# Performance work log

Measured on AMD Instinct MI355X. Metric: run time of the kernel, lower is better.

The kernel has to match this reference:

```python
import jax, jax.numpy as jnp
import numpy as np

N, E, U, L = 10000, 320000, 256, 3


def setup_inputs() -> dict:
    key = jax.random.key(0)
    ks = jax.random.split(key, 16)
    s = 0.05
    p = {}
    p["pos"] = jax.random.normal(ks[0], (N, 2), jnp.float32)
    p["edge_attr_in"] = jax.random.uniform(ks[1], (E, 1), jnp.float32)
    p["edge_index"] = jax.random.randint(ks[2], (2, E), 0, N)
    p["Wp"] = jax.random.normal(ks[3], (2, U), jnp.float32) * s
    p["bp"] = jnp.zeros((U,), jnp.float32)
    p["Wa"] = jax.random.normal(ks[4], (1, U), jnp.float32) * s
    p["ba"] = jnp.zeros((U,), jnp.float32)
    p["W1"] = jax.random.normal(ks[5], (L, U, U), jnp.float32) * s
    p["b1"] = jnp.zeros((L, U), jnp.float32)
    p["W2"] = jax.random.normal(ks[6], (L, U, U), jnp.float32) * s
    p["b2"] = jnp.zeros((L, U), jnp.float32)
    p["We"] = jax.random.normal(ks[7], (L + 1, U, U), jnp.float32) * s
    p["be"] = jnp.zeros((L + 1, U), jnp.float32)
    p["Ws"] = jax.random.normal(ks[8], (L + 1, U, U), jnp.float32) * s
    p["Wt"] = jax.random.normal(ks[9], (L + 1, U, U), jnp.float32) * s
    p["Wm1"] = jax.random.normal(ks[10], (U + 1, U // 2), jnp.float32) * s
    p["bm1"] = jnp.zeros((U // 2,), jnp.float32)
    p["alpha"] = 0.25 * jnp.ones((1,), jnp.float32)  # PReLU default slope
    p["Wm2"] = jax.random.normal(ks[11], (U // 2, 1), jnp.float32) * s
    p["bm2"] = jnp.zeros((1,), jnp.float32)
    return p


def _forward(pos, edge_attr_in, edge_index, Wp, bp, Wa, ba, W1, b1, W2, b2,
             We, be, Ws, Wt, Wm1, bm1, alpha, Wm2, bm2):
    src, dst = edge_index[0], edge_index[1]
    x = pos @ Wp + bp                      # [N, U]
    e = edge_attr_in @ Wa + ba             # [E, U]

    def edge_update(x, e, l):
        # ResEdgeLinear: residual edge update from endpoint nodes + edge feats
        return e + jax.nn.relu(e @ We[l] + x[src] @ Ws[l] + x[dst] @ Wt[l] + be[l])

    for l in range(L):
        # ResNodeConv: gated gather-linear-scatter with residual
        gate = jax.nn.sigmoid(e)                                   # [E, U]
        msg = gate * (x[src] @ W2[l] + b2[l])                      # [E, U]
        agg = jax.ops.segment_sum(msg, dst, num_segments=N)        # [N, U]
        x_new = x + jax.nn.relu(x @ W1[l] + b1[l] + agg)
        e_new = edge_update(x, e, l)  # simultaneous update: both use old (x, e)
        x, e = x_new, e_new
    e = edge_update(x, e, L)

    h = jnp.concatenate([e, edge_attr_in[:, :1]], axis=-1) @ Wm1 + bm1
    h = jnp.where(h > 0, h, alpha * h)  # PReLU
    return h @ Wm2 + bm2                # [E, 1] logits


def reference(pos, edge_attr_in, edge_index, Wp, bp, Wa, ba, W1, b1, W2, b2,
              We, be, Ws, Wt, Wm1, bm1, alpha, Wm2, bm2):
    return _forward(pos, edge_attr_in, edge_index, Wp, bp, Wa, ba, W1, b1,
                    W2, b2, We, be, Ws, Wt, Wm1, bm1, alpha, Wm2, bm2)
```

## Files before the change

### kernel.cpp

```cpp
#include <hip/hip_runtime.h>
#include <stdint.h>

#define N_NODES 10000
#define N_EDGES 320000

using bf16x8 = __attribute__((ext_vector_type(8))) short;
using fp32x4 = __attribute__((ext_vector_type(4))) float;
using u16x8 = __attribute__((ext_vector_type(8))) unsigned short;
using i32x4 = __attribute__((ext_vector_type(4))) int;

__device__ __forceinline__ float bf2f(unsigned short u) {
  union { unsigned int i; float f; } v; v.i = ((unsigned int)u) << 16; return v.f;
}
__device__ __forceinline__ unsigned short f2bf(float f) {
  union { float f; unsigned int i; } v; v.f = f;
  unsigned int x = v.i;
  x += 0x7fffu + ((x >> 16) & 1u);
  return (unsigned short)(x >> 16);
}

#define A_POS 0
#define A_EA 20000
#define A_WP 340000
#define A_BP 340512
#define A_WA 340768
#define A_BA 341024
#define A_W1 341280
#define A_B1 537888
#define A_W2 538656
#define A_B2 735264
#define A_WE 736032
#define A_BE 998176
#define A_WS 999200
#define A_WT 1261344
#define A_WM1 1523488
#define A_BM1 1556384
#define A_AL 1556512
#define A_WM2 1556544
#define A_BM2 1556672
#define ARENA_USED 1556673
#define ARENA_TOT 1556736

__constant__ int g_off[19] = {A_POS, A_EA, A_WP, A_BP, A_WA, A_BA, A_W1, A_B1,
                              A_W2, A_B2, A_WE, A_BE, A_WS, A_WT, A_WM1,
                              A_BM1, A_AL, A_WM2, A_BM2};

struct Ptrs { const void* p[19]; };

__global__ void k_detect(const unsigned short* wpraw, int* flag, int* deg) {
  int i = blockIdx.x * 256 + threadIdx.x;
  if (i < N_NODES) deg[i] = 0;
  if (blockIdx.x == 0) {
    __shared__ int cnt;
    int tid = threadIdx.x;
    if (tid == 0) cnt = 0;
    __syncthreads();
    float v0 = bf2f(wpraw[tid]);
    float v1 = bf2f(wpraw[256 + tid]);
    int big = (fabsf(v0) > 100.f ? 1 : 0) + (fabsf(v1) > 100.f ? 1 : 0);
    atomicAdd(&cnt, big);
    __syncthreads();
    if (tid == 0) *flag = (cnt > 10) ? 1 : 0;
  }
}

__global__ void k_cast(Ptrs ptrs, const int* __restrict__ flag,
                       unsigned short* __restrict__ arena) {
  int a = blockIdx.x * 256 + threadIdx.x;
  if (a >= ARENA_USED) return;
  int z = 0;
#pragma unroll
  for (int j = 1; j < 19; ++j) if (a >= g_off[j]) z = j;
  int i = a - g_off[z];
  float v;
  if (*flag) v = ((const float*)ptrs.p[z])[i];
  else       v = bf2f(((const unsigned short*)ptrs.p[z])[i]);
  arena[a] = f2bf(v);
}

__global__ void k_prep(const unsigned short* __restrict__ arena,
                       unsigned short* nodeBT, unsigned short* WeT,
                       unsigned short* Wm1T, unsigned short* biascat) {
  int z = blockIdx.z;
  int i = blockIdx.x * 256 + threadIdx.x;
  if (z == 19) {
    if (i < 3072) {
      int l = i >> 10, j = i & 1023;
      unsigned short v = 0;
      if (j < 256) v = arena[A_B1 + l * 256 + j];
      else if (j < 512) v = arena[A_B2 + l * 256 + (j - 256)];
      biascat[i] = v;
    } else if (i < 3584) {
      biascat[i] = 0;
    }
    return;
  }
  const unsigned short* src; unsigned short* dst; int srcN = 256;
  if (z < 3)       {                 src = arena + A_W1 + z * 65536; dst = nodeBT + z * 262144; }
  else if (z < 6)  { int l = z - 3;  src = arena + A_W2 + l * 65536; dst = nodeBT + l * 262144 + 65536; }
  else if (z < 10) { int l = z - 6;  src = arena + A_WS + l * 65536;
                     dst = (l < 3) ? nodeBT + l * 262144 + 131072 : nodeBT + 786432; }
  else if (z < 14) { int l = z - 10; src = arena + A_WT + l * 65536;
                     dst = (l < 3) ? nodeBT + l * 262144 + 196608 : nodeBT + 786432 + 65536; }
  else if (z < 18) { int l = z - 14; src = arena + A_WE + l * 65536; dst = WeT + l * 65536; }
  else             { src = arena + A_WM1; dst = Wm1T; srcN = 128; }
  if (i < srcN * 256) {
    int k = i & 255, n = i >> 8;
    dst[i] = src[k * srcN + n];
  }
}

__global__ void k_init_x(const unsigned short* __restrict__ arena,
                         float* __restrict__ xf, unsigned short* __restrict__ xbf,
                         float* __restrict__ agg) {
  int n = blockIdx.x, c = threadIdx.x;
  float p0 = bf2f(arena[A_POS + 2 * n]), p1 = bf2f(arena[A_POS + 2 * n + 1]);
  float v = fmaf(p0, bf2f(arena[A_WP + c]),
                 fmaf(p1, bf2f(arena[A_WP + 256 + c]), bf2f(arena[A_BP + c])));
  long idx = ((long)n << 8) + c;
  xf[idx] = v;
  xbf[idx] = f2bf(v);
  agg[idx] = 0.f;
}

__global__ void k_hist(const int* __restrict__ dstA, int* __restrict__ deg) {
  int i = blockIdx.x * 256 + threadIdx.x;
  if (i < N_EDGES) {
    int d = dstA[i];
    if ((unsigned)d < N_NODES) atomicAdd(&deg[d], 1);
  }
}

__global__ void k_scan(const int* __restrict__ deg, int* __restrict__ rowptr,
                       int* __restrict__ cursor) {
  __shared__ int part[256];
  int tid = threadIdx.x;
  int base = tid * 40;
  int s = 0;
  for (int i = 0; i < 40; ++i) {
    int idx = base + i;
    if (idx < N_NODES) s += deg[idx];
  }
  part[tid] = s;
  __syncthreads();
  if (tid == 0) {
    int run = 0;
    for (int i = 0; i < 256; ++i) { int t = part[i]; part[i] = run; run += t; }
    rowptr[N_NODES] = run;
  }
  __syncthreads();
  int run = part[tid];
  for (int i = 0; i < 40; ++i) {
    int idx = base + i;
    if (idx < N_NODES) { rowptr[idx] = run; cursor[idx] = run; run += deg[idx]; }
  }
}

__global__ void k_fill(const int* __restrict__ dstA, const int* __restrict__ srcA,
                       const unsigned short* __restrict__ arena,
                       int* __restrict__ cursor, int* __restrict__ eid,
                       int* __restrict__ csrc, int* __restrict__ cdst,
                       unsigned short* __restrict__ eaC) {
  int i = blockIdx.x * 256 + threadIdx.x;
  if (i < N_EDGES) {
    int d = dstA[i]; if ((unsigned)d >= N_NODES) d = 0;
    int p = atomicAdd(&cursor[d], 1);
    if ((unsigned)p < N_EDGES) {
      eid[p] = i;
      int s = srcA[i]; if ((unsigned)s >= N_NODES) s = 0;
      csrc[p] = s;
      cdst[p] = d;
      eaC[p] = arena[A_EA + i];
    }
  }
}

#define SM_PITCH 528
#define EDGE_BLOCKS (N_EDGES / 128)

template <bool NT, int ROWS>
__device__ __forceinline__ void stage_tile(char* smc, const unsigned short* src,
                                           long rowBase) {
  int tid = threadIdx.x;
#pragma unroll
  for (int it = 0; it < ROWS / 8; ++it) {
    int lin = it * 256 + tid;
    int row = lin >> 5, g = lin & 31;
    const i32x4* p = (const i32x4*)((const char*)src + ((rowBase + row) << 9) + (g << 4));
    i32x4 v = NT ? __builtin_nontemporal_load(p) : *p;
    *(i32x4*)(smc + row * SM_PITCH + (g << 4)) = v;
  }
}

template <int MT, int NTT>
__device__ __forceinline__ void gemm_swap(const char* smc, const unsigned short* WT,
                                          int colBase, fp32x4 (&acc)[MT][NTT]) {
  const int lane = threadIdx.x & 63;
  const int q = lane >> 4, ll = lane & 15;
  const int llperm = ((ll >> 2) * (MT * 4)) + (ll & 3);
#pragma unroll
  for (int ks = 0; ks < 8; ++ks) {
    bf16x8 a[MT];
#pragma unroll
    for (int mt = 0; mt < MT; ++mt) {
      int oc = colBase + llperm + mt * 4;
      a[mt] = *(const bf16x8*)((const char*)WT + ((long)oc << 9) + (ks << 6) + (q << 4));
    }
    bf16x8 b[NTT];
#pragma unroll
    for (int nt = 0; nt < NTT; ++nt)
      b[nt] = *(const bf16x8*)(smc + (nt * 16 + ll) * SM_PITCH + (ks << 6) + (q << 4));
#pragma unroll
    for (int mt = 0; mt < MT; ++mt)
#pragma unroll
      for (int nt = 0; nt < NTT; ++nt)
        acc[mt][nt] = __builtin_amdgcn_mfma_f32_16x16x32_bf16(a[mt], b[nt], acc[mt][nt], 0, 0, 0);
  }
}

template <int NTT>
__device__ __forceinline__ void edge_epilogue(
    char* smc, const fp32x4 (&acc)[4][NTT], const int* s_src, const int* s_dst,
    const unsigned short* XW, int xw_pitch, int xs_off, int xt_off,
    const unsigned short* bePtr, int cb, int ll) {
  u16x8 be0 = *(const u16x8*)(bePtr + cb);
  u16x8 be1 = *(const u16x8*)(bePtr + cb + 8);
#pragma unroll
  for (int nt = 0; nt < NTT; ++nt) {
    int el = nt * 16 + ll;
    int sn = s_src[el], dn = s_dst[el];
    const unsigned short* xsrow = XW + (long)sn * xw_pitch + xs_off + cb;
    const unsigned short* xtrow = XW + (long)dn * xw_pitch + xt_off + cb;
    u16x8 xs0 = *(const u16x8*)(xsrow);
    u16x8 xs1 = *(const u16x8*)(xsrow + 8);
    u16x8 xt0 = *(const u16x8*)(xtrow);
    u16x8 xt1 = *(const u16x8*)(xtrow + 8);
    u16x8* slot = (u16x8*)(smc + el * SM_PITCH + cb * 2);
    u16x8 er0 = slot[0], er1 = slot[1];
    u16x8 o0, o1;
#pragma unroll
    for (int mt = 0; mt < 4; ++mt)
#pragma unroll
      for (int r = 0; r < 4; ++r) {
        int i = mt * 4 + r;
        float xsv = bf2f(i < 8 ? xs0[i] : xs1[i - 8]);
        float xtv = bf2f(i < 8 ? xt0[i] : xt1[i - 8]);
        float erv = bf2f(i < 8 ? er0[i] : er1[i - 8]);
        float bev = bf2f(i < 8 ? be0[i] : be1[i - 8]);
        float v = acc[mt][nt][r] + xsv + xtv + bev;
        v = fmaxf(v, 0.f);
        unsigned short ob = f2bf(erv + v);
        if (i < 8) o0[i] = ob; else o1[i - 8] = ob;
      }
    slot[0] = o0;
    slot[1] = o1;
  }
}

template <int MODE>
__global__ __launch_bounds__(256, 2) void k_fat(
    unsigned short* __restrict__ e, const unsigned short* __restrict__ WT_edge,
    const unsigned short* __restrict__ XW_edge,
    const unsigned short* __restrict__ bePtr, const unsigned short* __restrict__ arena,
    const unsigned short* __restrict__ eaC,
    const int* __restrict__ csrc, const int* __restrict__ cdst,
    const unsigned short* __restrict__ xbf, const unsigned short* __restrict__ WT_node,
    const unsigned short* __restrict__ bias, unsigned short* __restrict__ XW_out) {
  __shared__ int4 sm4[128 * 33];
  __shared__ int s_src[128];
  __shared__ int s_dst[128];
  char* smc = (char*)sm4;
  const int tid = threadIdx.x;
  const int wave = tid >> 6, lane = tid & 63;
  const int q = lane >> 4, ll = lane & 15;

  if (blockIdx.x < EDGE_BLOCKS) {
    const long tileBase = (long)blockIdx.x * 128;
    const int colBase = wave * 64;
    if (MODE == 0) {
#pragma unroll
      for (int it = 0; it < 16; ++it) {
        int lin = it * 256 + tid;
        int row = lin >> 5, g = lin & 31;
        float eav = bf2f(eaC[tileBase + row]);
        int c0 = g * 8;
        bf16x8 ov;
#pragma unroll
        for (int j = 0; j < 8; ++j) {
          float f = fmaf(eav, bf2f(arena[A_WA + c0 + j]), bf2f(arena[A_BA + c0 + j]));
          ((unsigned short*)&ov)[j] = f2bf(f);
        }
        *(bf16x8*)(smc + row * SM_PITCH + (g << 4)) = ov;
      }
    } else {
      stage_tile<true, 128>(smc, e, tileBase);
    }
    if (tid < 128) {
      long edge = tileBase + tid;
      int s = csrc[edge]; if ((unsigned)s >= N_NODES) s = 0;
      int d = cdst[edge]; if ((unsigned)d >= N_NODES) d = 0;
      s_src[tid] = s;
      s_dst[tid] = d;
    }
    __syncthreads();

    fp32x4 acc[4][8];
#pragma unroll
    for (int mt = 0; mt < 4; ++mt)
#pragma unroll
      for (int nt = 0; nt < 8; ++nt) acc[mt][nt] = 0.f;
    gemm_swap<4, 8>(smc, WT_edge, colBase, acc);
    __syncthreads();

    edge_epilogue<8>(smc, acc, s_src, s_dst, XW_edge, 1024, 512, 768,
                     bePtr, colBase + q * 16, ll);
    __syncthreads();

#pragma unroll
    for (int it = 0; it < 16; ++it) {
      int lin = it * 256 + tid;
      int row = lin >> 5, g = lin & 31;
      i32x4 v = *(const i32x4*)(smc + row * SM_PITCH + (g << 4));
      __builtin_nontemporal_store(v, (i32x4*)((char*)e + ((tileBase + row) << 9) + (g << 4)));
    }
  } else {
    int b = blockIdx.x - EDGE_BLOCKS;
    int bx = b % 79, by = b / 79;
    const long tileBase = (long)bx * 128;
#pragma unroll
    for (int it = 0; it < 16; ++it) {
      int lin = it * 256 + tid;
      int row = lin >> 5, g = lin & 31;
      long rg = tileBase + row;
      if (rg > N_NODES - 1) rg = N_NODES - 1;
      i32x4 v = *(const i32x4*)((const char*)xbf + (rg << 9) + (g << 4));
      *(i32x4*)(smc + row * SM_PITCH + (g << 4)) = v;
    }
    __syncthreads();
    fp32x4 acc[2][8];
#pragma unroll
    for (int mt = 0; mt < 2; ++mt)
#pragma unroll
      for (int nt = 0; nt < 8; ++nt) acc[mt][nt] = 0.f;
    const int colBase = by * 128 + wave * 32;
    gemm_swap<2, 8>(smc, WT_node, colBase, acc);

    const int cb = colBase + q * 8;
    u16x8 bs8 = *(const u16x8*)(bias + cb);
#pragma unroll
    for (int nt = 0; nt < 8; ++nt) {
      long nn = tileBase + nt * 16 + ll;
      if (nn >= N_NODES) continue;
      u16x8 o0;
#pragma unroll
      for (int mt = 0; mt < 2; ++mt)
#pragma unroll
        for (int r = 0; r < 4; ++r) {
          int i = mt * 4 + r;
          o0[i] = f2bf(acc[mt][nt][r] + bf2f(bs8[i]));
        }
      *(u16x8*)(XW_out + nn * 1024 + cb) = o0;
    }
  }
}

__global__ __launch_bounds__(256, 2) void k_edge_last2(
    const unsigned short* __restrict__ e, const unsigned short* __restrict__ WeT2,
    const unsigned short* __restrict__ WeT3,
    const unsigned short* __restrict__ XW2, const unsigned short* __restrict__ XW3,
    const unsigned short* __restrict__ arena, const unsigned short* __restrict__ eaC,
    const int* __restrict__ csrc, const int* __restrict__ cdst,
    const unsigned short* __restrict__ Wm1T, const int* __restrict__ eid,
    const int* __restrict__ flag, void* __restrict__ out) {
  __shared__ int4 sm4[128 * 33];
  __shared__ int s_src[128];
  __shared__ int s_dst[128];
  char* smc = (char*)sm4;
  const long tileBase = (long)blockIdx.x * 128;
  const int tid = threadIdx.x;
  const int wave = tid >> 6, lane = tid & 63;
  const int q = lane >> 4, ll = lane & 15;
  const int colBase = wave * 64;

  stage_tile<true, 128>(smc, e, tileBase);
  if (tid < 128) {
    long edge = tileBase + tid;
    int s = csrc[edge]; if ((unsigned)s >= N_NODES) s = 0;
    int d = cdst[edge]; if ((unsigned)d >= N_NODES) d = 0;
    s_src[tid] = s;
    s_dst[tid] = d;
  }
  __syncthreads();

  fp32x4 acc[4][8];
#pragma unroll
  for (int mt = 0; mt < 4; ++mt)
#pragma unroll
    for (int nt = 0; nt < 8; ++nt) acc[mt][nt] = 0.f;
  gemm_swap<4, 8>(smc, WeT2, colBase, acc);
  __syncthreads();
  edge_epilogue<8>(smc, acc, s_src, s_dst, XW2, 1024, 512, 768,
                   arena + A_BE + 2 * 256, colBase + q * 16, ll);
  __syncthreads();

#pragma unroll
  for (int mt = 0; mt < 4; ++mt)
#pragma unroll
    for (int nt = 0; nt < 8; ++nt) acc[mt][nt] = 0.f;
  gemm_swap<4, 8>(smc, WeT3, colBase, acc);
  __syncthreads();
  edge_epilogue<8>(smc, acc, s_src, s_dst, XW3, 512, 0, 256,
                   arena + A_BE + 3 * 256, colBase + q * 16, ll);
  __syncthreads();

  fp32x4 acc2[2][8];
#pragma unroll
  for (int mt = 0; mt < 2; ++mt)
#pragma unroll
    for (int nt = 0; nt < 8; ++nt) acc2[mt][nt] = 0.f;
  const int colBase2 = wave * 32;
  gemm_swap<2, 8>(smc, Wm1T, colBase2, acc2);

  const int cb2 = colBase2 + q * 8;
  float alphaf = bf2f(arena[A_AL]);
  float bmc[8], wl[8], w2c[8];
#pragma unroll
  for (int i = 0; i < 8; ++i) {
    bmc[i] = bf2f(arena[A_BM1 + cb2 + i]);
    wl[i] = bf2f(arena[A_WM1 + 32768 + cb2 + i]);
    w2c[i] = bf2f(arena[A_WM2 + cb2 + i]);
  }
  __syncthreads();
  float* part = (float*)smc;
#pragma unroll
  for (int nt = 0; nt < 8; ++nt) {
    int el = nt * 16 + ll;
    float eav = bf2f(eaC[tileBase + el]);
    float ps = 0.f;
#pragma unroll
    for (int mt = 0; mt < 2; ++mt)
#pragma unroll
      for (int r = 0; r < 4; ++r) {
        int i = mt * 4 + r;
        float h = acc2[mt][nt][r] + bmc[i] + eav * wl[i];
        h = (h > 0.f) ? h : alphaf * h;
        ps += h * w2c[i];
      }
    ps += __shfl_xor(ps, 16, 64);
    ps += __shfl_xor(ps, 32, 64);
    if (q == 0) part[el * 4 + wave] = ps;
  }
  __syncthreads();
  if (tid < 128) {
    float t = part[tid * 4] + part[tid * 4 + 1] + part[tid * 4 + 2] + part[tid * 4 + 3]
            + bf2f(arena[A_BM2]);
    long row = tileBase + tid;
    int oe = eid[row]; if ((unsigned)oe >= N_EDGES) oe = 0;
    if (*flag) ((float*)out)[oe] = t;
    else       ((unsigned short*)out)[oe] = f2bf(t);
  }
}

__global__ __launch_bounds__(256, 2) void k_node_gemm(
    const unsigned short* __restrict__ xbf, const unsigned short* __restrict__ WT,
    const unsigned short* __restrict__ bias, unsigned short* __restrict__ out,
    int out_pitch) {
  __shared__ int4 sm4[128 * 33];
  char* smc = (char*)sm4;
  const long tileBase = (long)blockIdx.x * 128;
  {
    int tid = threadIdx.x;
#pragma unroll
    for (int it = 0; it < 16; ++it) {
      int lin = it * 256 + tid;
      int row = lin >> 5, g = lin & 31;
      long rg = tileBase + row;
      if (rg > N_NODES - 1) rg = N_NODES - 1;
      i32x4 v = *(const i32x4*)((const char*)xbf + (rg << 9) + (g << 4));
      *(i32x4*)(smc + row * SM_PITCH + (g << 4)) = v;
    }
  }
  __syncthreads();
  fp32x4 acc[2][8];
#pragma unroll
  for (int mt = 0; mt < 2; ++mt)
#pragma unroll
    for (int nt = 0; nt < 8; ++nt) acc[mt][nt] = 0.f;
  const int tid = threadIdx.x, wave = tid >> 6, lane = tid & 63;
  const int q = lane >> 4, ll = lane & 15;
  const int colBase = blockIdx.y * 128 + wave * 32;
  gemm_swap<2, 8>(smc, WT, colBase, acc);

  const int cb = colBase + q * 8;
  u16x8 bs8 = *(const u16x8*)(bias + cb);
#pragma unroll
  for (int nt = 0; nt < 8; ++nt) {
    long nn = tileBase + nt * 16 + ll;
    if (nn >= N_NODES) continue;
    u16x8 o0;
#pragma unroll
    for (int mt = 0; mt < 2; ++mt)
#pragma unroll
      for (int r = 0; r < 4; ++r) {
        int i = mt * 4 + r;
        o0[i] = f2bf(acc[mt][nt][r] + bf2f(bs8[i]));
      }
    *(u16x8*)(out + nn * out_pitch + cb) = o0;
  }
}

template <bool FIRST>
__global__ void k_agg(const int* __restrict__ csrc, const int* __restrict__ cdst,
                      const unsigned short* __restrict__ e,
                      const unsigned short* __restrict__ eaC,
                      const unsigned short* __restrict__ arena,
                      const unsigned short* __restrict__ XW, int xw_pitch, int x2_off,
                      float* __restrict__ agg) {
  __shared__ int s_src[64];
  __shared__ int s_dst[64];
  const long base = (long)blockIdx.x * 64;
  const int c = threadIdx.x;
  if (c < 64) {
    long r = base + c;
    int s = csrc[r]; if ((unsigned)s >= N_NODES) s = 0;
    int d = cdst[r]; if ((unsigned)d >= N_NODES) d = 0;
    s_src[c] = s;
    s_dst[c] = d;
  }
  __syncthreads();
  float wac = 0.f, bac = 0.f;
  if (FIRST) { wac = bf2f(arena[A_WA + c]); bac = bf2f(arena[A_BA + c]); }
  float a = 0.f;
  int run = s_dst[0];
  for (int b8 = 0; b8 < 64; b8 += 8) {
    float evv[8], x2v[8];
#pragma unroll
    for (int j = 0; j < 8; ++j) {
      int row = b8 + j;
      if (FIRST) evv[j] = fmaf(bf2f(eaC[base + row]), wac, bac);
      else evv[j] = bf2f(__builtin_nontemporal_load(e + ((base + row) << 8) + c));
      x2v[j] = bf2f(XW[(long)s_src[row] * xw_pitch + x2_off + c]);
    }
#pragma unroll
    for (int j = 0; j < 8; ++j) {
      int d = s_dst[b8 + j];
      if (d != run) {
        atomicAdd(&agg[((long)run << 8) + c], a);
        a = 0.f;
        run = d;
      }
      float gate = 1.f / (1.f + __expf(-evv[j]));
      a = fmaf(gate, x2v[j], a);
    }
  }
  atomicAdd(&agg[((long)run << 8) + c], a);
}

__global__ void k_node_update(float* __restrict__ xf, unsigned short* __restrict__ xbf,
                              const unsigned short* __restrict__ XW,
                              float* __restrict__ agg) {
  int n = blockIdx.x, c = threadIdx.x;
  long idx = ((long)n << 8) + c;
  float av = agg[idx];
  agg[idx] = 0.f;
  float t = bf2f(XW[((long)n << 10) + c]) + av;
  float nx = xf[idx] + fmaxf(t, 0.f);
  xf[idx] = nx;
  xbf[idx] = f2bf(nx);
}

extern "C" void kernel_launch(void* const* d_in, const int* in_sizes, int n_in,
                              void* d_out, int out_size, void* d_ws, size_t ws_size,
                              hipStream_t stream) {
  const int* eidx = (const int*)d_in[2];
  const int* srcA = eidx;
  const int* dstA = eidx + N_EDGES;
  (void)in_sizes; (void)n_in; (void)out_size;

  char* ws = (char*)d_ws;
  size_t off = 0;
  auto alloc = [&](size_t bytes) -> char* {
    char* p = ws + off;
    off = (off + bytes + 255) & ~(size_t)255;
    return p;
  };
  unsigned short* e_buf   = (unsigned short*)alloc((size_t)N_EDGES * 256 * 2);
  float*          xf      = (float*)alloc((size_t)N_NODES * 256 * 4);
  unsigned short* xbf     = (unsigned short*)alloc((size_t)N_NODES * 256 * 2);
  unsigned short* XWa     = (unsigned short*)alloc((size_t)N_NODES * 1024 * 2);
  unsigned short* XWb     = (unsigned short*)alloc((size_t)N_NODES * 1024 * 2);
  unsigned short* XW3     = (unsigned short*)alloc((size_t)N_NODES * 512 * 2);
  float*          agg     = (float*)alloc((size_t)N_NODES * 256 * 4);
  unsigned short* nodeBT  = (unsigned short*)alloc((size_t)917504 * 2);
  unsigned short* WeT     = (unsigned short*)alloc((size_t)4 * 65536 * 2);
  unsigned short* Wm1T    = (unsigned short*)alloc((size_t)32768 * 2);
  unsigned short* biascat = (unsigned short*)alloc((size_t)3584 * 2);
  unsigned short* arena   = (unsigned short*)alloc((size_t)ARENA_TOT * 2);
  int* deg    = (int*)alloc((size_t)N_NODES * 4);
  int* rowptr = (int*)alloc((size_t)(N_NODES + 1) * 4);
  int* cursor = (int*)alloc((size_t)N_NODES * 4);
  int* eid    = (int*)alloc((size_t)N_EDGES * 4);
  int* csrc   = (int*)alloc((size_t)N_EDGES * 4);
  int* cdst   = (int*)alloc((size_t)N_EDGES * 4);
  unsigned short* eaC = (unsigned short*)alloc((size_t)N_EDGES * 2);
  int* flag   = (int*)alloc(4);
  if (ws_size < off) return;

  Ptrs ptrs;
  {
    int map[19] = {0, 1, 3, 4, 5, 6, 7, 8, 9, 10, 11, 12, 13, 14, 15, 16, 17, 18, 19};
    for (int j = 0; j < 19; ++j) ptrs.p[j] = d_in[map[j]];
  }

  dim3 blk(256);
  k_detect<<<dim3(40), blk, 0, stream>>>((const unsigned short*)d_in[3], flag, deg);
  k_cast<<<dim3((ARENA_USED + 255) / 256), blk, 0, stream>>>(ptrs, flag, arena);
  k_prep<<<dim3(256, 1, 20), blk, 0, stream>>>(arena, nodeBT, WeT, Wm1T, biascat);
  k_init_x<<<dim3(N_NODES), blk, 0, stream>>>(arena, xf, xbf, agg);
  k_hist<<<dim3(N_EDGES / 256), blk, 0, stream>>>(dstA, deg);
  k_scan<<<dim3(1), blk, 0, stream>>>(deg, rowptr, cursor);
  k_fill<<<dim3(N_EDGES / 256), blk, 0, stream>>>(dstA, srcA, arena, cursor, eid, csrc,
                                                  cdst, eaC);

  k_node_gemm<<<dim3(79, 8), blk, 0, stream>>>(xbf, nodeBT, biascat, XWa, 1024);
  k_agg<true><<<dim3(N_EDGES / 64), blk, 0, stream>>>(csrc, cdst, e_buf, eaC, arena,
                                                      XWa, 1024, 256, agg);
  k_node_update<<<dim3(N_NODES), blk, 0, stream>>>(xf, xbf, XWa, agg);
  k_fat<0><<<dim3(EDGE_BLOCKS + 632), blk, 0, stream>>>(
      e_buf, WeT, XWa, arena + A_BE, arena, eaC, csrc, cdst,
      xbf, nodeBT + 262144, biascat + 1024, XWb);
  k_agg<false><<<dim3(N_EDGES / 64), blk, 0, stream>>>(csrc, cdst, e_buf, eaC, arena,
                                                       XWb, 1024, 256, agg);
  k_node_update<<<dim3(N_NODES), blk, 0, stream>>>(xf, xbf, XWb, agg);
  k_fat<1><<<dim3(EDGE_BLOCKS + 632), blk, 0, stream>>>(
      e_buf, WeT + 65536, XWb, arena + A_BE + 256, arena, eaC, csrc, cdst,
      xbf, nodeBT + 2 * 262144, biascat + 2048, XWa);
  k_agg<false><<<dim3(N_EDGES / 64), blk, 0, stream>>>(csrc, cdst, e_buf, eaC, arena,
                                                       XWa, 1024, 256, agg);
  k_node_update<<<dim3(N_NODES), blk, 0, stream>>>(xf, xbf, XWa, agg);
  k_node_gemm<<<dim3(79, 4), blk, 0, stream>>>(xbf, nodeBT + 786432, biascat + 3072, XW3, 512);
  k_edge_last2<<<dim3(EDGE_BLOCKS), blk, 0, stream>>>(
      e_buf, WeT + 2 * 65536, WeT + 3 * 65536, XWa, XW3, arena, eaC,
      csrc, cdst, Wm1T, eid, flag, d_out);
}
```

Baseline: 870.9 us.

## Pre-pack weights in MFMA fragment order and stage source-node rows through LDS

Adds a packing kernel that reorders the transposed weight matrices into the per-lane MFMA fragment order, so each weight load in the GEMM inner loop becomes a contiguous 1KB per-wave access instead of scattered 16-byte row reads. The edge epilogue now gathers source-node XW rows cooperatively, with each lane loading one 16-byte chunk and prefetching the next tile. The gathered rows are written to a per-wave LDS scratch and then read back in the MFMA output layout. The cost is three extra small launches, duplicate weight buffers, and about 9KB more LDS per block, which could reduce occupancy.

```diff
diff --git a/kernel.cpp b/kernel.cpp
--- a/kernel.cpp
+++ b/kernel.cpp
@@ -110,6 +110,21 @@
   }
 }
 
+__global__ void k_pack(const unsigned short* __restrict__ src,
+                       unsigned short* __restrict__ dst, int MT, int nchunks) {
+  int c = blockIdx.x * 256 + threadIdx.x;
+  if (c >= nchunks) return;
+  int perg = MT * 512;
+  int g = c / perg, r = c % perg;
+  int ks = r / (64 * MT);
+  int rem = r % (64 * MT);
+  int mt = rem >> 6, lane = rem & 63;
+  int q = lane >> 4, ll = lane & 15;
+  int oc = g * (MT * 16) + (ll >> 2) * (MT * 4) + (ll & 3) + mt * 4;
+  i32x4 v = *(const i32x4*)((const char*)src + ((long)oc << 9) + (ks << 6) + (q << 4));
+  ((i32x4*)dst)[c] = v;
+}
+
 __global__ void k_init_x(const unsigned short* __restrict__ arena,
                          float* __restrict__ xf, unsigned short* __restrict__ xbf,
                          float* __restrict__ agg) {
@@ -176,15 +191,16 @@
 }
 
 #define SM_PITCH 528
+#define XS_PITCH 144
 #define EDGE_BLOCKS (N_EDGES / 128)
 
-template <bool NT, int ROWS>
+template <bool NT, int ROWS, int BLK>
 __device__ __forceinline__ void stage_tile(char* smc, const unsigned short* src,
                                            long rowBase) {
   int tid = threadIdx.x;
 #pragma unroll
-  for (int it = 0; it < ROWS / 8; ++it) {
-    int lin = it * 256 + tid;
+  for (int it = 0; it < ROWS * 32 / BLK; ++it) {
+    int lin = it * BLK + tid;
     int row = lin >> 5, g = lin & 31;
     const i32x4* p = (const i32x4*)((const char*)src + ((rowBase + row) << 9) + (g << 4));
     i32x4 v = NT ? __builtin_nontemporal_load(p) : *p;
@@ -193,19 +209,17 @@
 }
 
 template <int MT, int NTT>
-__device__ __forceinline__ void gemm_swap(const char* smc, const unsigned short* WT,
+__device__ __forceinline__ void gemm_swap(const char* smc, const unsigned short* WTp,
                                           int colBase, fp32x4 (&acc)[MT][NTT]) {
   const int lane = threadIdx.x & 63;
   const int q = lane >> 4, ll = lane & 15;
-  const int llperm = ((ll >> 2) * (MT * 4)) + (ll & 3);
+  const char* wbase = (const char*)WTp + ((long)colBase << 9) + (lane << 4);
 #pragma unroll
   for (int ks = 0; ks < 8; ++ks) {
     bf16x8 a[MT];
 #pragma unroll
-    for (int mt = 0; mt < MT; ++mt) {
-      int oc = colBase + llperm + mt * 4;
-      a[mt] = *(const bf16x8*)((const char*)WT + ((long)oc << 9) + (ks << 6) + (q << 4));
-    }
+    for (int mt = 0; mt < MT; ++mt)
+      a[mt] = *(const bf16x8*)(wbase + ((long)(ks * MT + mt) << 10));
     bf16x8 b[NTT];
 #pragma unroll
     for (int nt = 0; nt < NTT; ++nt)
@@ -219,22 +233,35 @@
 }
 
 template <int NTT>
-__device__ __forceinline__ void edge_epilogue(
-    char* smc, const fp32x4 (&acc)[4][NTT], const int* s_src, const int* s_dst,
-    const unsigned short* XW, int xw_pitch, int xs_off, int xt_off,
-    const unsigned short* bePtr, int cb, int ll) {
+__device__ __forceinline__ void edge_epilogue_cx(
+    char* smc, char* xsw, const fp32x4 (&acc)[4][NTT], const int* s_src,
+    const int* s_dst, const unsigned short* XW, int xw_pitch, int xs_off,
+    int xt_off, const unsigned short* bePtr, int colBase, int lane) {
+  const int q = lane >> 4, ll = lane & 15;
+  const int cb = colBase + q * 16;
   u16x8 be0 = *(const u16x8*)(bePtr + cb);
   u16x8 be1 = *(const u16x8*)(bePtr + cb + 8);
+  const int prow = lane >> 3;
+  const int ppc = lane & 7;
+  const int pcol = xs_off + colBase + ppc * 8;
+  u16x8 pfA = *(const u16x8*)(XW + (long)s_src[prow] * xw_pitch + pcol);
+  u16x8 pfB = *(const u16x8*)(XW + (long)s_src[8 + prow] * xw_pitch + pcol);
 #pragma unroll
   for (int nt = 0; nt < NTT; ++nt) {
+    *(u16x8*)(xsw + prow * XS_PITCH + ppc * 16) = pfA;
+    *(u16x8*)(xsw + (8 + prow) * XS_PITCH + ppc * 16) = pfB;
+    if (nt + 1 < NTT) {
+      int elA = (nt + 1) * 16 + prow;
+      pfA = *(const u16x8*)(XW + (long)s_src[elA] * xw_pitch + pcol);
+      pfB = *(const u16x8*)(XW + (long)s_src[elA + 8] * xw_pitch + pcol);
+    }
     int el = nt * 16 + ll;
-    int sn = s_src[el], dn = s_dst[el];
-    const unsigned short* xsrow = XW + (long)sn * xw_pitch + xs_off + cb;
+    int dn = s_dst[el];
     const unsigned short* xtrow = XW + (long)dn * xw_pitch + xt_off + cb;
-    u16x8 xs0 = *(const u16x8*)(xsrow);
-    u16x8 xs1 = *(const u16x8*)(xsrow + 8);
     u16x8 xt0 = *(const u16x8*)(xtrow);
     u16x8 xt1 = *(const u16x8*)(xtrow + 8);
+    u16x8 xs0 = *(const u16x8*)(xsw + ll * XS_PITCH + q * 32);
+    u16x8 xs1 = *(const u16x8*)(xsw + ll * XS_PITCH + q * 32 + 16);
     u16x8* slot = (u16x8*)(smc + el * SM_PITCH + cb * 2);
     u16x8 er0 = slot[0], er1 = slot[1];
     u16x8 o0, o1;
@@ -267,6 +294,7 @@
     const unsigned short* __restrict__ xbf, const unsigned short* __restrict__ WT_node,
     const unsigned short* __restrict__ bias, unsigned short* __restrict__ XW_out) {
   __shared__ int4 sm4[128 * 33];
+  __shared__ int4 xsb4[4 * 2304 / 16];
   __shared__ int s_src[128];
   __shared__ int s_dst[128];
   char* smc = (char*)sm4;
@@ -293,7 +321,7 @@
         *(bf16x8*)(smc + row * SM_PITCH + (g << 4)) = ov;
       }
     } else {
-      stage_tile<true, 128>(smc, e, tileBase);
+      stage_tile<true, 128, 256>(smc, e, tileBase);
     }
     if (tid < 128) {
       long edge = tileBase + tid;
@@ -312,8 +340,8 @@
     gemm_swap<4, 8>(smc, WT_edge, colBase, acc);
     __syncthreads();
 
-    edge_epilogue<8>(smc, acc, s_src, s_dst, XW_edge, 1024, 512, 768,
-                     bePtr, colBase + q * 16, ll);
+    edge_epilogue_cx<8>(smc, (char*)xsb4 + wave * 2304, acc, s_src, s_dst,
+                        XW_edge, 1024, 512, 768, bePtr, colBase, lane);
     __syncthreads();
 
 #pragma unroll
@@ -373,6 +401,7 @@
     const unsigned short* __restrict__ Wm1T, const int* __restrict__ eid,
     const int* __restrict__ flag, void* __restrict__ out) {
   __shared__ int4 sm4[128 * 33];
+  __shared__ int4 xsb4[4 * 2304 / 16];
   __shared__ int s_src[128];
   __shared__ int s_dst[128];
   char* smc = (char*)sm4;
@@ -381,8 +410,9 @@
   const int wave = tid >> 6, lane = tid & 63;
   const int q = lane >> 4, ll = lane & 15;
   const int colBase = wave * 64;
-
-  stage_tile<true, 128>(smc, e, tileBase);
+  char* xsw = (char*)xsb4 + wave * 2304;
+
+  stage_tile<true, 128, 256>(smc, e, tileBase);
   if (tid < 128) {
     long edge = tileBase + tid;
     int s = csrc[edge]; if ((unsigned)s >= N_NODES) s = 0;
@@ -399,8 +429,8 @@
     for (int nt = 0; nt < 8; ++nt) acc[mt][nt] = 0.f;
   gemm_swap<4, 8>(smc, WeT2, colBase, acc);
   __syncthreads();
-  edge_epilogue<8>(smc, acc, s_src, s_dst, XW2, 1024, 512, 768,
-                   arena + A_BE + 2 * 256, colBase + q * 16, ll);
+  edge_epilogue_cx<8>(smc, xsw, acc, s_src, s_dst, XW2, 1024, 512, 768,
+                      arena + A_BE + 2 * 256, colBase, lane);
   __syncthreads();
 
 #pragma unroll
@@ -409,8 +439,8 @@
     for (int nt = 0; nt < 8; ++nt) acc[mt][nt] = 0.f;
   gemm_swap<4, 8>(smc, WeT3, colBase, acc);
   __syncthreads();
-  edge_epilogue<8>(smc, acc, s_src, s_dst, XW3, 512, 0, 256,
-                   arena + A_BE + 3 * 256, colBase + q * 16, ll);
+  edge_epilogue_cx<8>(smc, xsw, acc, s_src, s_dst, XW3, 512, 0, 256,
+                      arena + A_BE + 3 * 256, colBase, lane);
   __syncthreads();
 
   fp32x4 acc2[2][8];
@@ -594,6 +624,9 @@
   unsigned short* nodeBT  = (unsigned short*)alloc((size_t)917504 * 2);
   unsigned short* WeT     = (unsigned short*)alloc((size_t)4 * 65536 * 2);
   unsigned short* Wm1T    = (unsigned short*)alloc((size_t)32768 * 2);
+  unsigned short* nodeBTp = (unsigned short*)alloc((size_t)917504 * 2);
+  unsigned short* WeTp    = (unsigned short*)alloc((size_t)4 * 65536 * 2);
+  unsigned short* Wm1Tp   = (unsigned short*)alloc((size_t)32768 * 2);
   unsigned short* biascat = (unsigned short*)alloc((size_t)3584 * 2);
   unsigned short* arena   = (unsigned short*)alloc((size_t)ARENA_TOT * 2);
   int* deg    = (int*)alloc((size_t)N_NODES * 4);
@@ -616,30 +649,33 @@
   k_detect<<<dim3(40), blk, 0, stream>>>((const unsigned short*)d_in[3], flag, deg);
   k_cast<<<dim3((ARENA_USED + 255) / 256), blk, 0, stream>>>(ptrs, flag, arena);
   k_prep<<<dim3(256, 1, 20), blk, 0, stream>>>(arena, nodeBT, WeT, Wm1T, biascat);
+  k_pack<<<dim3(448), blk, 0, stream>>>(nodeBT, nodeBTp, 2, 114688);
+  k_pack<<<dim3(128), blk, 0, stream>>>(WeT, WeTp, 4, 32768);
+  k_pack<<<dim3(16),  blk, 0, stream>>>(Wm1T, Wm1Tp, 2, 4096);
   k_init_x<<<dim3(N_NODES), blk, 0, stream>>>(arena, xf, xbf, agg);
   k_hist<<<dim3(N_EDGES / 256), blk, 0, stream>>>(dstA, deg);
   k_scan<<<dim3(1), blk, 0, stream>>>(deg, rowptr, cursor);
   k_fill<<<dim3(N_EDGES / 256), blk, 0, stream>>>(dstA, srcA, arena, cursor, eid, csrc,
                                                   cdst, eaC);
 
-  k_node_gemm<<<dim3(79, 8), blk, 0, stream>>>(xbf, nodeBT, biascat, XWa, 1024);
+  k_node_gemm<<<dim3(79, 8), blk, 0, stream>>>(xbf, nodeBTp, biascat, XWa, 1024);
   k_agg<true><<<dim3(N_EDGES / 64), blk, 0, stream>>>(csrc, cdst, e_buf, eaC, arena,
                                                       XWa, 1024, 256, agg);
   k_node_update<<<dim3(N_NODES), blk, 0, stream>>>(xf, xbf, XWa, agg);
   k_fat<0><<<dim3(EDGE_BLOCKS + 632), blk, 0, stream>>>(
-      e_buf, WeT, XWa, arena + A_BE, arena, eaC, csrc, cdst,
-      xbf, nodeBT + 262144, biascat + 1024, XWb);
+      e_buf, WeTp, XWa, arena + A_BE, arena, eaC, csrc, cdst,
+      xbf, nodeBTp + 262144, biascat + 1024, XWb);
   k_agg<false><<<dim3(N_EDGES / 64), blk, 0, stream>>>(csrc, cdst, e_buf, eaC, arena,
                                                        XWb, 1024, 256, agg);
   k_node_update<<<dim3(N_NODES), blk, 0, stream>>>(xf, xbf, XWb, agg);
   k_fat<1><<<dim3(EDGE_BLOCKS + 632), blk, 0, stream>>>(
-      e_buf, WeT + 65536, XWb, arena + A_BE + 256, arena, eaC, csrc, cdst,
-      xbf, nodeBT + 2 * 262144, biascat + 2048, XWa);
+      e_buf, WeTp + 65536, XWb, arena + A_BE + 256, arena, eaC, csrc, cdst,
+      xbf, nodeBTp + 2 * 262144, biascat + 2048, XWa);
   k_agg<false><<<dim3(N_EDGES / 64), blk, 0, stream>>>(csrc, cdst, e_buf, eaC, arena,
                                                        XWa, 1024, 256, agg);
   k_node_update<<<dim3(N_NODES), blk, 0, stream>>>(xf, xbf, XWa, agg);
-  k_node_gemm<<<dim3(79, 4), blk, 0, stream>>>(xbf, nodeBT + 786432, biascat + 3072, XW3, 512);
+  k_node_gemm<<<dim3(79, 4), blk, 0, stream>>>(xbf, nodeBTp + 786432, biascat + 3072, XW3, 512);
   k_edge_last2<<<dim3(EDGE_BLOCKS), blk, 0, stream>>>(
-      e_buf, WeT + 2 * 65536, WeT + 3 * 65536, XWa, XW3, arena, eaC,
-      csrc, cdst, Wm1T, eid, flag, d_out);
-}
+      e_buf, WeTp + 2 * 65536, WeTp + 3 * 65536, XWa, XW3, arena, eaC,
+      csrc, cdst, Wm1Tp, eid, flag, d_out);
+}
```

New measurement: 821.1 us. -5.7%, faster.
